# Performance work log

Measured on AMD Instinct MI355X. Metric: run time of the kernel, lower is better.

## Reference

```python
import jax, jax.numpy as jnp
import numpy as np

VOCAB, EMB, HID, OUT, T, B = 50000, 512, 1024, 1, 256, 256


def setup_inputs() -> dict:
    key = jax.random.key(0)
    ks = jax.random.split(key, 8)
    s_ih = 1.0 / np.sqrt(HID)
    return {
        "text": jax.random.randint(ks[0], (B, T), 0, VOCAB, dtype=jnp.int64),
        "emb": jax.random.normal(ks[1], (VOCAB, EMB), jnp.float32),
        "w_ih": jax.random.uniform(ks[2], (4 * HID, EMB), jnp.float32, -s_ih, s_ih),
        "w_hh": jax.random.uniform(ks[3], (4 * HID, HID), jnp.float32, -s_ih, s_ih),
        "b_ih": jax.random.uniform(ks[4], (4 * HID,), jnp.float32, -s_ih, s_ih),
        "b_hh": jax.random.uniform(ks[5], (4 * HID,), jnp.float32, -s_ih, s_ih),
        "fc_w": jax.random.uniform(ks[6], (OUT, HID), jnp.float32, -s_ih, s_ih),
        "fc_b": jax.random.uniform(ks[7], (OUT,), jnp.float32, -s_ih, s_ih),
    }


def _lstm_last_hidden(x, w_ih, w_hh, b_ih, b_hh):
    # x: [B, T, E]. Precompute input contribution to all gates: [B, T, 4H].
    xg = jnp.einsum("bte,ge->btg", x, w_ih) + b_ih + b_hh
    Bn = x.shape[0]
    H = w_hh.shape[1]
    h0 = jnp.zeros((Bn, H), x.dtype)
    c0 = jnp.zeros((Bn, H), x.dtype)

    def step(carry, xt):
        h, c = carry
        gates = xt + h @ w_hh.T  # [B, 4H], PyTorch gate order i,f,g,o
        i, f, g, o = jnp.split(gates, 4, axis=-1)
        c = jax.nn.sigmoid(f) * c + jax.nn.sigmoid(i) * jnp.tanh(g)
        h = jax.nn.sigmoid(o) * jnp.tanh(c)
        return (h, c), None

    (h, c), _ = jax.lax.scan(step, (h0, c0), jnp.swapaxes(xg, 0, 1))
    return h  # last hidden state [B, H]


def reference(text, emb, w_ih, w_hh, b_ih, b_hh, fc_w, fc_b):
    x = emb[text]  # [B, T, E]
    h = _lstm_last_hidden(x, w_ih, w_hh, b_ih, b_hh)
    return jax.nn.sigmoid(h @ fc_w.T + fc_b)  # [B, OUT]
```

## Files before the change

kernel.cpp:

```cpp
#include <hip/hip_runtime.h>

#define TT 256
#define BB 256
#define EE 512
#define HH 1024
#define G4 4096
#define KTOT 1536
#define BK 128
#define APAD 8

typedef __attribute__((ext_vector_type(8))) short short8;
typedef __attribute__((ext_vector_type(4))) float f32x4;

__device__ __forceinline__ short f2bf(float f) {
    unsigned u; __builtin_memcpy(&u, &f, 4);
    unsigned r = (u + 0x7FFFu + ((u >> 16) & 1u)) >> 16;
    return (short)(unsigned short)r;
}
__device__ __forceinline__ float bf2f(short s) {
    unsigned u = ((unsigned)(unsigned short)s) << 16;
    float f; __builtin_memcpy(&f, &u, 4);
    return f;
}
__device__ __forceinline__ float sigf(float x) { return 1.f / (1.f + __expf(-x)); }

__global__ __launch_bounds__(256) void prep_kernel(
    const float* __restrict__ w_ih, const float* __restrict__ w_hh,
    const float* __restrict__ b_ih, const float* __restrict__ b_hh,
    short* __restrict__ w_cat, float* __restrict__ bias)
{
    int r = blockIdx.x;
    int tid = threadIdx.x;
    for (int c = tid; c < KTOT; c += 256) {
        float v = (c < HH) ? w_hh[(size_t)r * HH + c]
                           : w_ih[(size_t)r * EE + (c - HH)];
        w_cat[(size_t)r * KTOT + c] = f2bf(v);
    }
    if (tid == 0) bias[r] = b_ih[r] + b_hh[r];
}

__global__ __launch_bounds__(256) void gather_kernel(
    const int* __restrict__ text, const float* __restrict__ emb,
    short* __restrict__ xbf)
{
    int row = blockIdx.x * 4 + (threadIdx.x >> 6);
    int b = row >> 8, t = row & 255;
    int lane = threadIdx.x & 63;
    int v = text[row];
    const float* src = emb + (size_t)v * EE + lane * 8;
    float4 f0 = *(const float4*)src;
    float4 f1 = *(const float4*)(src + 4);
    float fv[8];
    *(float4*)&fv[0] = f0; *(float4*)&fv[4] = f1;
    short8 s;
    #pragma unroll
    for (int i = 0; i < 8; ++i) s[i] = f2bf(fv[i]);
    *(short8*)(xbf + ((size_t)t * BB + b) * EE + lane * 8) = s;
}

__global__ __launch_bounds__(256) void lstm_step(
    const short* __restrict__ w_cat,
    const float* __restrict__ bias,
    const short* __restrict__ xbf,
    const short* __restrict__ h_in,
    short*       __restrict__ h_out,
    float*       __restrict__ c_st,
    int t)
{
    __shared__ short At[2][64][BK + APAD];
    __shared__ float Gt[4][64][17];

    const int tid  = threadIdx.x;
    const int wv   = tid >> 6;
    const int lane = tid & 63;
    const int n    = lane & 15;
    const int q    = lane >> 4;

    const int bid = blockIdx.x;
    const int xcd = bid & 7, sub = bid >> 3;
    const int j0  = (xcd * 8 + (sub & 7)) * 16;
    const int b0  = (sub >> 3) * 64;

    const short* wrow = w_cat + (size_t)(wv * HH + j0 + n) * KTOT;

    const int ar = tid >> 2;
    const int ac = (tid & 3) * 32;
    const int ab = b0 + ar;
    const short* hrow = h_in + (size_t)ab * HH;
    const short* xrow = xbf + ((size_t)t * BB + ab) * EE - HH;

    const int kstart = (t == 0) ? HH : 0;
    const int niter  = (KTOT - kstart) / BK;

    f32x4 acc[4];
    #pragma unroll
    for (int i = 0; i < 4; ++i) acc[i] = (f32x4){0.f, 0.f, 0.f, 0.f};

    {
        const short* s = ((kstart < HH) ? hrow : xrow) + kstart + ac;
        *(short8*)&At[0][ar][ac]      = *(const short8*)(s);
        *(short8*)&At[0][ar][ac + 8]  = *(const short8*)(s + 8);
        *(short8*)&At[0][ar][ac + 16] = *(const short8*)(s + 16);
        *(short8*)&At[0][ar][ac + 24] = *(const short8*)(s + 24);
    }
    __syncthreads();

    for (int i = 0; i < niter; ++i) {
        const int k0  = kstart + i * BK;
        const int cur = i & 1;
        const bool more = (i + 1 < niter);
        short8 r0, r1, r2, r3;
        if (more) {
            const int kn = k0 + BK;
            const short* s = ((kn < HH) ? hrow : xrow) + kn + ac;
            r0 = *(const short8*)(s);
            r1 = *(const short8*)(s + 8);
            r2 = *(const short8*)(s + 16);
            r3 = *(const short8*)(s + 24);
        }
        #pragma unroll
        for (int ks = 0; ks < 4; ++ks) {
            short8 bfrag = *(const short8*)(wrow + k0 + ks * 32 + q * 8);
            #pragma unroll
            for (int mt = 0; mt < 4; ++mt) {
                short8 afrag = *(const short8*)&At[cur][mt * 16 + n][ks * 32 + q * 8];
                acc[mt] = __builtin_amdgcn_mfma_f32_16x16x32_bf16(afrag, bfrag, acc[mt], 0, 0, 0);
            }
        }
        if (more) {
            *(short8*)&At[cur ^ 1][ar][ac]      = r0;
            *(short8*)&At[cur ^ 1][ar][ac + 8]  = r1;
            *(short8*)&At[cur ^ 1][ar][ac + 16] = r2;
            *(short8*)&At[cur ^ 1][ar][ac + 24] = r3;
            __syncthreads();
        }
    }

    #pragma unroll
    for (int mt = 0; mt < 4; ++mt)
        #pragma unroll
        for (int r = 0; r < 4; ++r)
            Gt[wv][mt * 16 + q * 4 + r][n] = acc[mt][r];
    __syncthreads();

    const int m  = tid >> 2;
    const int n4 = (tid & 3) * 4;
    const int b  = b0 + m;
    #pragma unroll
    for (int u = 0; u < 4; ++u) {
        const int nn = n4 + u;
        const int j  = j0 + nn;
        float ip = Gt[0][m][nn] + bias[j];
        float fp = Gt[1][m][nn] + bias[HH + j];
        float gp = Gt[2][m][nn] + bias[2 * HH + j];
        float op = Gt[3][m][nn] + bias[3 * HH + j];
        float co = (t == 0) ? 0.f : c_st[(size_t)b * HH + j];
        float cn = sigf(fp) * co + sigf(ip) * tanhf(gp);
        float hn = sigf(op) * tanhf(cn);
        c_st[(size_t)b * HH + j] = cn;
        h_out[(size_t)b * HH + j] = f2bf(hn);
    }
}

__global__ __launch_bounds__(256) void fc_kernel(
    const short* __restrict__ hbuf, const float* __restrict__ fc_w,
    const float* __restrict__ fc_b, float* __restrict__ out)
{
    __shared__ float red[4];
    int b = blockIdx.x;
    int tid = threadIdx.x;
    float s = 0.f;
    for (int k = tid; k < HH; k += 256)
        s += bf2f(hbuf[(size_t)b * HH + k]) * fc_w[k];
    #pragma unroll
    for (int off = 32; off > 0; off >>= 1) s += __shfl_down(s, off);
    if ((tid & 63) == 0) red[tid >> 6] = s;
    __syncthreads();
    if (tid == 0) {
        float tot = red[0] + red[1] + red[2] + red[3] + fc_b[0];
        out[b] = 1.f / (1.f + __expf(-tot));
    }
}

extern "C" void kernel_launch(void* const* d_in, const int* in_sizes, int n_in,
                              void* d_out, int out_size, void* d_ws, size_t ws_size,
                              hipStream_t stream) {
    const int*   text = (const int*)d_in[0];
    const float* emb  = (const float*)d_in[1];
    const float* w_ih = (const float*)d_in[2];
    const float* w_hh = (const float*)d_in[3];
    const float* b_ih = (const float*)d_in[4];
    const float* b_hh = (const float*)d_in[5];
    const float* fc_w = (const float*)d_in[6];
    const float* fc_b = (const float*)d_in[7];
    float* out = (float*)d_out;

    char* ws = (char*)d_ws;
    short* w_cat = (short*)(ws);
    float* bias  = (float*)(ws + 12582912);
    short* xbf   = (short*)(ws + 12599296);
    short* hbuf0 = (short*)(ws + 79708160);
    short* hbuf1 = (short*)(ws + 80232448);
    float* c_st  = (float*)(ws + 80756736);

    gather_kernel<<<dim3(BB * TT / 4), dim3(256), 0, stream>>>(text, emb, xbf);
    prep_kernel<<<dim3(G4), dim3(256), 0, stream>>>(w_ih, w_hh, b_ih, b_hh, w_cat, bias);

    for (int t = 0; t < TT; ++t) {
        const short* hin  = (t & 1) ? hbuf1 : hbuf0;
        short*       hout = (t & 1) ? hbuf0 : hbuf1;
        lstm_step<<<dim3(256), dim3(256), 0, stream>>>(
            w_cat, bias, xbf, hin, hout, c_st, t);
    }

    fc_kernel<<<dim3(BB), dim3(256), 0, stream>>>(hbuf0, fc_w, fc_b, out);
}
```

Before: 4.910 ms.

## Fuse timestep loop into persistent cooperative kernel with register-resident cell state

Replaces the 256 per-timestep kernel launches with one cooperative kernel that loops over time and uses grid.sync between steps. The cell state now stays in registers, bias loads are hoisted out of the loop, h is written as a short4 vector, and tanh/sigmoid use rcp-based fast approximations. This is meant to remove launch overhead and the global c_st traffic. In exchange it adds grid-wide barrier cost, relies on all 256 blocks being co-resident, and slightly changes numerics.

```diff
diff --git a/kernel.cpp b/kernel.cpp
--- a/kernel.cpp
+++ b/kernel.cpp
@@ -1,4 +1,7 @@
 #include <hip/hip_runtime.h>
+#include <hip/hip_cooperative_groups.h>
+
+namespace cg = cooperative_groups;
 
 #define TT 256
 #define BB 256
@@ -10,6 +13,7 @@
 #define APAD 8
 
 typedef __attribute__((ext_vector_type(8))) short short8;
+typedef __attribute__((ext_vector_type(4))) short short4v;
 typedef __attribute__((ext_vector_type(4))) float f32x4;
 
 __device__ __forceinline__ short f2bf(float f) {
@@ -22,7 +26,12 @@
     float f; __builtin_memcpy(&f, &u, 4);
     return f;
 }
-__device__ __forceinline__ float sigf(float x) { return 1.f / (1.f + __expf(-x)); }
+__device__ __forceinline__ float sigf(float x) {
+    return __builtin_amdgcn_rcpf(1.f + __expf(-x));
+}
+__device__ __forceinline__ float tanh_fast(float x) {
+    return 2.f * sigf(x + x) - 1.f;
+}
 
 __global__ __launch_bounds__(256) void prep_kernel(
     const float* __restrict__ w_ih, const float* __restrict__ w_hh,
@@ -58,15 +67,15 @@
     *(short8*)(xbf + ((size_t)t * BB + b) * EE + lane * 8) = s;
 }
 
-__global__ __launch_bounds__(256) void lstm_step(
+__global__ __launch_bounds__(256) void lstm_seq(
     const short* __restrict__ w_cat,
     const float* __restrict__ bias,
     const short* __restrict__ xbf,
-    const short* __restrict__ h_in,
-    short*       __restrict__ h_out,
-    float*       __restrict__ c_st,
-    int t)
-{
+    short*       __restrict__ hbuf0,
+    short*       __restrict__ hbuf1)
+{
+    cg::grid_group grid = cg::this_grid();
+
     __shared__ short At[2][64][BK + APAD];
     __shared__ float Gt[4][64][17];
 
@@ -86,79 +95,97 @@
     const int ar = tid >> 2;
     const int ac = (tid & 3) * 32;
     const int ab = b0 + ar;
-    const short* hrow = h_in + (size_t)ab * HH;
-    const short* xrow = xbf + ((size_t)t * BB + ab) * EE - HH;
-
-    const int kstart = (t == 0) ? HH : 0;
-    const int niter  = (KTOT - kstart) / BK;
-
-    f32x4 acc[4];
+    const short* hrow0 = hbuf0 + (size_t)ab * HH;
+    const short* hrow1 = hbuf1 + (size_t)ab * HH;
+    const short* xrow  = xbf + (size_t)ab * EE - HH;
+
+    const int m   = tid >> 2;
+    const int n4  = (tid & 3) * 4;
+    const int jb  = j0 + n4;
+    const int eb  = b0 + m;
+    float bi0[4], bf1[4], bg2[4], bo3[4];
     #pragma unroll
-    for (int i = 0; i < 4; ++i) acc[i] = (f32x4){0.f, 0.f, 0.f, 0.f};
-
-    {
-        const short* s = ((kstart < HH) ? hrow : xrow) + kstart + ac;
-        *(short8*)&At[0][ar][ac]      = *(const short8*)(s);
-        *(short8*)&At[0][ar][ac + 8]  = *(const short8*)(s + 8);
-        *(short8*)&At[0][ar][ac + 16] = *(const short8*)(s + 16);
-        *(short8*)&At[0][ar][ac + 24] = *(const short8*)(s + 24);
-    }
-    __syncthreads();
-
-    for (int i = 0; i < niter; ++i) {
-        const int k0  = kstart + i * BK;
-        const int cur = i & 1;
-        const bool more = (i + 1 < niter);
-        short8 r0, r1, r2, r3;
-        if (more) {
-            const int kn = k0 + BK;
-            const short* s = ((kn < HH) ? hrow : xrow) + kn + ac;
-            r0 = *(const short8*)(s);
-            r1 = *(const short8*)(s + 8);
-            r2 = *(const short8*)(s + 16);
-            r3 = *(const short8*)(s + 24);
+    for (int u = 0; u < 4; ++u) {
+        bi0[u] = bias[jb + u];
+        bf1[u] = bias[HH + jb + u];
+        bg2[u] = bias[2 * HH + jb + u];
+        bo3[u] = bias[3 * HH + jb + u];
+    }
+    float creg[4] = {0.f, 0.f, 0.f, 0.f};
+    short* hout_even = hbuf1 + (size_t)eb * HH + jb;
+    short* hout_odd  = hbuf0 + (size_t)eb * HH + jb;
+
+    for (int t = 0; t < TT; ++t) {
+        const short* hrow  = (t & 1) ? hrow1 : hrow0;
+        const int kstart   = (t == 0) ? HH : 0;
+        const int niter    = (KTOT - kstart) >> 7;
+
+        f32x4 acc[4];
+        #pragma unroll
+        for (int i = 0; i < 4; ++i) acc[i] = (f32x4){0.f, 0.f, 0.f, 0.f};
+
+        {
+            const short* s = ((kstart < HH) ? hrow : xrow) + kstart + ac;
+            *(short8*)&At[0][ar][ac]      = *(const short8*)(s);
+            *(short8*)&At[0][ar][ac + 8]  = *(const short8*)(s + 8);
+            *(short8*)&At[0][ar][ac + 16] = *(const short8*)(s + 16);
+            *(short8*)&At[0][ar][ac + 24] = *(const short8*)(s + 24);
         }
-        #pragma unroll
-        for (int ks = 0; ks < 4; ++ks) {
-            short8 bfrag = *(const short8*)(wrow + k0 + ks * 32 + q * 8);
+        __syncthreads();
+
+        for (int i = 0; i < niter; ++i) {
+            const int k0  = kstart + (i << 7);
+            const int cur = i & 1;
+            const bool more = (i + 1 < niter);
+            short8 r0, r1, r2, r3;
+            if (more) {
+                const int kn = k0 + BK;
+                const short* s = ((kn < HH) ? hrow : xrow) + kn + ac;
+                r0 = *(const short8*)(s);
+                r1 = *(const short8*)(s + 8);
+                r2 = *(const short8*)(s + 16);
+                r3 = *(const short8*)(s + 24);
+            }
             #pragma unroll
-            for (int mt = 0; mt < 4; ++mt) {
-                short8 afrag = *(const short8*)&At[cur][mt * 16 + n][ks * 32 + q * 8];
-                acc[mt] = __builtin_amdgcn_mfma_f32_16x16x32_bf16(afrag, bfrag, acc[mt], 0, 0, 0);
+            for (int ks = 0; ks < 4; ++ks) {
+                short8 bfrag = *(const short8*)(wrow + k0 + ks * 32 + q * 8);
+                #pragma unroll
+                for (int mt = 0; mt < 4; ++mt) {
+                    short8 afrag = *(const short8*)&At[cur][mt * 16 + n][ks * 32 + q * 8];
+                    acc[mt] = __builtin_amdgcn_mfma_f32_16x16x32_bf16(afrag, bfrag, acc[mt], 0, 0, 0);
+                }
+            }
+            if (more) {
+                *(short8*)&At[cur ^ 1][ar][ac]      = r0;
+                *(short8*)&At[cur ^ 1][ar][ac + 8]  = r1;
+                *(short8*)&At[cur ^ 1][ar][ac + 16] = r2;
+                *(short8*)&At[cur ^ 1][ar][ac + 24] = r3;
+                __syncthreads();
             }
         }
-        if (more) {
-            *(short8*)&At[cur ^ 1][ar][ac]      = r0;
-            *(short8*)&At[cur ^ 1][ar][ac + 8]  = r1;
-            *(short8*)&At[cur ^ 1][ar][ac + 16] = r2;
-            *(short8*)&At[cur ^ 1][ar][ac + 24] = r3;
-            __syncthreads();
+
+        #pragma unroll
+        for (int mt = 0; mt < 4; ++mt)
+            #pragma unroll
+            for (int r = 0; r < 4; ++r)
+                Gt[wv][mt * 16 + q * 4 + r][n] = acc[mt][r];
+        __syncthreads();
+
+        short4v hv;
+        #pragma unroll
+        for (int u = 0; u < 4; ++u) {
+            float ip = Gt[0][m][n4 + u] + bi0[u];
+            float fp = Gt[1][m][n4 + u] + bf1[u];
+            float gp = Gt[2][m][n4 + u] + bg2[u];
+            float op = Gt[3][m][n4 + u] + bo3[u];
+            float cn = sigf(fp) * creg[u] + sigf(ip) * tanh_fast(gp);
+            creg[u]  = cn;
+            hv[u]    = f2bf(sigf(op) * tanh_fast(cn));
         }
-    }
-
-    #pragma unroll
-    for (int mt = 0; mt < 4; ++mt)
-        #pragma unroll
-        for (int r = 0; r < 4; ++r)
-            Gt[wv][mt * 16 + q * 4 + r][n] = acc[mt][r];
-    __syncthreads();
-
-    const int m  = tid >> 2;
-    const int n4 = (tid & 3) * 4;
-    const int b  = b0 + m;
-    #pragma unroll
-    for (int u = 0; u < 4; ++u) {
-        const int nn = n4 + u;
-        const int j  = j0 + nn;
-        float ip = Gt[0][m][nn] + bias[j];
-        float fp = Gt[1][m][nn] + bias[HH + j];
-        float gp = Gt[2][m][nn] + bias[2 * HH + j];
-        float op = Gt[3][m][nn] + bias[3 * HH + j];
-        float co = (t == 0) ? 0.f : c_st[(size_t)b * HH + j];
-        float cn = sigf(fp) * co + sigf(ip) * tanhf(gp);
-        float hn = sigf(op) * tanhf(cn);
-        c_st[(size_t)b * HH + j] = cn;
-        h_out[(size_t)b * HH + j] = f2bf(hn);
+        *(short4v*)((t & 1) ? hout_odd : hout_even) = hv;
+
+        xrow += (size_t)BB * EE;
+        if (t + 1 < TT) grid.sync();
     }
 }
 
@@ -201,17 +228,18 @@
     short* xbf   = (short*)(ws + 12599296);
     short* hbuf0 = (short*)(ws + 79708160);
     short* hbuf1 = (short*)(ws + 80232448);
-    float* c_st  = (float*)(ws + 80756736);
 
     gather_kernel<<<dim3(BB * TT / 4), dim3(256), 0, stream>>>(text, emb, xbf);
     prep_kernel<<<dim3(G4), dim3(256), 0, stream>>>(w_ih, w_hh, b_ih, b_hh, w_cat, bias);
 
-    for (int t = 0; t < TT; ++t) {
-        const short* hin  = (t & 1) ? hbuf1 : hbuf0;
-        short*       hout = (t & 1) ? hbuf0 : hbuf1;
-        lstm_step<<<dim3(256), dim3(256), 0, stream>>>(
-            w_cat, bias, xbf, hin, hout, c_st, t);
-    }
+    const short* a0 = w_cat;
+    const float* a1 = bias;
+    const short* a2 = xbf;
+    short*       a3 = hbuf0;
+    short*       a4 = hbuf1;
+    void* args[] = { (void*)&a0, (void*)&a1, (void*)&a2, (void*)&a3, (void*)&a4 };
+    hipLaunchCooperativeKernel((const void*)lstm_seq, dim3(256), dim3(256),
+                               args, 0, stream);
 
     fc_kernel<<<dim3(BB), dim3(256), 0, stream>>>(hbuf0, fc_w, fc_b, out);
 }
```

Result: slower. 12.12 ms (+146.9%).
